# Optimization experiments

Measured on AMD Instinct MI355X. Metric: run time of the kernel, lower is better.

## Reference

```python
import jax, jax.numpy as jnp
import numpy as np

B, T, E = 8, 64, 512
H = 1024          # hidden_dim
OC = 2            # out_channels
VB = 32           # num_vel_bins
STEPS = 128


def setup_inputs() -> dict:
    key = jax.random.key(0)
    ks = jax.random.split(key, 16)
    s = 0.02
    f = lambda k, shp: jax.random.normal(k, shp, jnp.float32) * s
    return {
        "x": jax.random.normal(ks[0], (B, T, E), jnp.float32),
        "sos_token": f(ks[1], (1, 1, OC)),
        "Wc": f(ks[2], (E, H)), "bc": f(ks[3], (H,)),
        "Wi": f(ks[4], (OC, H)), "bi": f(ks[5], (H,)),
        "Wih0": f(ks[6], (2 * H, 4 * H)), "Whh0": f(ks[7], (H, 4 * H)),
        "bih0": f(ks[8], (4 * H,)), "bhh0": f(ks[9], (4 * H,)),
        "Wih1": f(ks[10], (H, 4 * H)), "Whh1": f(ks[11], (H, 4 * H)),
        "bih1": f(ks[12], (4 * H,)), "bhh1": f(ks[13], (4 * H,)),
        "Wo": f(ks[14], (H, 1 + VB)), "bo": f(ks[15], (1 + VB,)),
    }


def _lstm_cell(inp, h, c, Wih, Whh, b):
    # PyTorch gate order: i, f, g, o
    g = inp @ Wih + h @ Whh + b
    i, f, gg, o = jnp.split(g, 4, axis=-1)
    c = jax.nn.sigmoid(f) * c + jax.nn.sigmoid(i) * jnp.tanh(gg)
    h = jax.nn.sigmoid(o) * jnp.tanh(c)
    return h, c


def reference(x, sos_token, Wc, bc, Wi, bi, Wih0, Whh0, bih0, bhh0,
              Wih1, Whh1, bih1, bhh1, Wo, bo):
    Bx, Tx, Ex = x.shape
    BT = Bx * Tx
    Hd = Whh0.shape[0]
    nvb = Wo.shape[1] - 1
    cond = x.reshape(BT, Ex) @ Wc + bc            # [BT, H]
    b0 = bih0 + bhh0
    b1 = bih1 + bhh1
    z = jnp.zeros((BT, Hd), x.dtype)
    cur0 = jnp.broadcast_to(sos_token[0, 0], (BT, sos_token.shape[-1]))

    def step(carry, _):
        h0, c0, h1, c1, cur = carry
        inp = jnp.concatenate([cur @ Wi + bi, cond], axis=-1)  # [BT, 2H]
        h0, c0 = _lstm_cell(inp, h0, c0, Wih0, Whh0, b0)
        h1, c1 = _lstm_cell(h0, h1, c1, Wih1, Whh1, b1)
        logit = h1 @ Wo + bo                                   # [BT, 1+VB]
        pred_note = (jax.nn.sigmoid(logit[:, 0]) > 0.5).astype(x.dtype)
        pred_vel = jnp.argmax(logit[:, 1:], axis=-1).astype(x.dtype) / (nvb - 1.0)
        cur = jnp.stack([pred_note, pred_vel], axis=-1)        # [BT, 2]
        return (h0, c0, h1, c1, cur), logit

    _, logits = jax.lax.scan(step, (z, z, z, z, cur0), None, length=STEPS)
    # logits: [STEPS, BT, 1+VB] -> [B, 1+VB, T, 128]
    logits = logits.transpose(1, 0, 2).reshape(Bx, Tx, STEPS, 1 + nvb)
    return logits.transpose(0, 3, 1, 2)
```

## Files before the change

### kernel.cpp

```cpp
#include <hip/hip_runtime.h>
#include <hip/hip_bf16.h>


#define G4     4096
#define NSTEPS 128
#define NOUTC  33

typedef __attribute__((ext_vector_type(8))) short s8v;
typedef __attribute__((ext_vector_type(4))) float f4v;
typedef unsigned int u32;
typedef unsigned long long u64;

__device__ __forceinline__ float fsig(float x)  { return 1.0f / (1.0f + __expf(-x)); }
__device__ __forceinline__ float ftanh(float x) { return 2.0f / (1.0f + __expf(-2.0f * x)) - 1.0f; }

__device__ __forceinline__ short f2bf(float x) {
  union { __hip_bfloat16 b; short s; } u; u.b = __float2bfloat16(x); return u.s;
}
__device__ __forceinline__ float bf2f(short s) {
  union { __hip_bfloat16 b; short v; } u; u.v = s; return __bfloat162float(u.b);
}

__device__ __forceinline__ void gridbar(u32* bar, u32 target) {
  asm volatile("s_waitcnt vmcnt(0)" ::: "memory");
  __syncthreads();
  if (threadIdx.x == 0) {
    __hip_atomic_fetch_add(bar, 1u, __ATOMIC_RELAXED, __HIP_MEMORY_SCOPE_SYSTEM);
    while (__hip_atomic_load(bar, __ATOMIC_RELAXED, __HIP_MEMORY_SCOPE_SYSTEM) < target) {
      __builtin_amdgcn_s_sleep(1);
    }
  }
  __syncthreads();
}

__device__ __forceinline__ void stage16(short (*dst)[1032], const short* hbuf,
                                        int row0, int bankoff, int tid) {
#pragma unroll
  for (int i = 0; i < 8; ++i) {
    int q = i * 512 + tid;
    int row = q >> 8, c4 = q & 255;
    const u64* src = (const u64*)(hbuf + (size_t)(row0 + row) * G4 + bankoff) + c4;
    u64 v = __hip_atomic_load(src, __ATOMIC_RELAXED, __HIP_MEMORY_SCOPE_SYSTEM);
    *(u64*)&dst[row][c4 * 4] = v;
  }
}

__global__ __launch_bounds__(256) void transpose_frag_kernel(
    const float* __restrict__ src, short* __restrict__ dst_hi,
    short* __restrict__ dst_lo, int NK, int koff) {
  __shared__ float St[64][65];
  int n0 = (blockIdx.x & 63) * 64;
  int k0 = (blockIdx.x >> 6) * 64;
  int t = threadIdx.x;
  int nl = t & 63, kl = t >> 6;
#pragma unroll
  for (int it = 0; it < 16; ++it) {
    int k = kl + it * 4;
    St[k][nl] = src[(size_t)(k0 + k) * 4096 + n0 + nl];
  }
  __syncthreads();
  int lane = t & 63, w = t >> 6;
  for (int it = 0; it < 2; ++it) {
    int sub = it * 4 + w;
    int nt = sub >> 1, kc = sub & 1;
    int nloc = nt * 16 + (lane & 15);
    int kbase = kc * 32 + (lane >> 4) * 8;
    float v[8];
#pragma unroll
    for (int ii = 0; ii < 8; ++ii) v[ii] = St[kbase + ii][nloc];
    s8v hv;
#pragma unroll
    for (int ii = 0; ii < 8; ++ii) hv[ii] = f2bf(v[ii]);
    size_t ntg = (size_t)(n0 / 16 + nt);
    size_t kcg = (size_t)(k0 / 32 + kc + koff);
    size_t off = (ntg * (size_t)NK + kcg) * 512 + (size_t)lane * 8;
    *(s8v*)(dst_hi + off) = hv;
    if (dst_lo) {
      s8v lv;
#pragma unroll
      for (int ii = 0; ii < 8; ++ii) lv[ii] = f2bf(v[ii] - bf2f(hv[ii]));
      *(s8v*)(dst_lo + off) = lv;
    }
  }
}

__global__ __launch_bounds__(256) void cond_kernel(
    const float* __restrict__ x, const float* __restrict__ Wc,
    const float* __restrict__ bc, short* __restrict__ cond_hi,
    short* __restrict__ cond_lo) {
  __shared__ float xs[8][512];
  int rb = (blockIdx.x >> 2) * 8;
  int cb = (blockIdx.x & 3) * 256;
  int t = threadIdx.x;
  for (int i = t; i < 8 * 512; i += 256)
    xs[i >> 9][i & 511] = x[(size_t)(rb + (i >> 9)) * 512 + (i & 511)];
  __syncthreads();
  float acc[8] = {0, 0, 0, 0, 0, 0, 0, 0};
  for (int k = 0; k < 512; ++k) {
    float w = Wc[(size_t)k * 1024 + cb + t];
#pragma unroll
    for (int rr = 0; rr < 8; ++rr) acc[rr] += xs[rr][k] * w;
  }
  float bcv = bc[cb + t];
#pragma unroll
  for (int rr = 0; rr < 8; ++rr) {
    float v = acc[rr] + bcv;
    short hi = f2bf(v);
    cond_hi[(size_t)(rb + rr) * 1024 + cb + t] = hi;
    cond_lo[(size_t)(rb + rr) * 1024 + cb + t] = f2bf(v - bf2f(hi));
  }
}

__global__ __launch_bounds__(256) void vecs_kernel(
    const float* __restrict__ Wih0, const float* __restrict__ bi,
    const float* __restrict__ Wi, const float* __restrict__ bih0,
    const float* __restrict__ bhh0, const float* __restrict__ bih1,
    const float* __restrict__ bhh1, float* __restrict__ vec0,
    float* __restrict__ Wf, float* __restrict__ b1vec) {
  int n = blockIdx.x * 256 + threadIdx.x;
  float v0 = 0.f, w0 = 0.f, w1 = 0.f;
  for (int k = 0; k < 1024; ++k) {
    float w = Wih0[(size_t)k * 4096 + n];
    v0 += bi[k] * w;
    w0 += Wi[k] * w;
    w1 += Wi[1024 + k] * w;
  }
  vec0[n] = v0 + bih0[n] + bhh0[n];
  Wf[2 * n + 0] = w0;
  Wf[2 * n + 1] = w1;
  b1vec[n] = bih1[n] + bhh1[n];
}

__global__ __launch_bounds__(64) void wof_kernel(const float* __restrict__ Wo,
                                                 short* __restrict__ hi,
                                                 short* __restrict__ lo) {
  int nt = blockIdx.x >> 5;
  int kc = blockIdx.x & 31;
  int lane = threadIdx.x;
  int ch = nt * 16 + (lane & 15);
  int kb = kc * 32 + (lane >> 4) * 8;
  s8v hv, lv;
#pragma unroll
  for (int ii = 0; ii < 8; ++ii) {
    float v = (ch < NOUTC) ? Wo[(size_t)(kb + ii) * NOUTC + ch] : 0.f;
    short h = f2bf(v);
    hv[ii] = h;
    lv[ii] = f2bf(v - bf2f(h));
  }
  size_t off = ((size_t)(nt * 32 + kc)) * 512 + (size_t)lane * 8;
  *(s8v*)(hi + off) = hv;
  *(s8v*)(lo + off) = lv;
}

__global__ __launch_bounds__(512) void const0_kernel(
    const short* __restrict__ cond_hi, const short* __restrict__ cond_lo,
    const short* __restrict__ WTc_hi, const short* __restrict__ WTc_lo,
    const float* __restrict__ vec0, float* __restrict__ const0) {
  int j = blockIdx.x & 63, i = blockIdx.x >> 6;
  int w = threadIdx.x >> 6, lane = threadIdx.x & 63;
  int quad = lane >> 4, l16 = lane & 15;
  int rowA = i * 128 + w * 16 + l16;
  int rowC = i * 128 + w * 16 + quad * 4;
  int hid = j * 16 + l16;
  const short* ah = cond_hi + (size_t)rowA * 1024 + quad * 8;
  const short* al = cond_lo + (size_t)rowA * 1024 + quad * 8;
  f4v acc[4];
#pragma unroll
  for (int g = 0; g < 4; ++g) acc[g] = (f4v){0.f, 0.f, 0.f, 0.f};
#pragma unroll 2
  for (int kk = 0; kk < 32; ++kk) {
    s8v avh = *(const s8v*)(ah + kk * 32);
    s8v avl = *(const s8v*)(al + kk * 32);
#pragma unroll
    for (int g = 0; g < 4; ++g) {
      size_t off = ((size_t)(g * 64 + j) * 32 + kk) * 512 + (size_t)lane * 8;
      s8v bh = *(const s8v*)(WTc_hi + off);
      s8v bl = *(const s8v*)(WTc_lo + off);
      acc[g] = __builtin_amdgcn_mfma_f32_16x16x32_bf16(avh, bh, acc[g], 0, 0, 0);
      acc[g] = __builtin_amdgcn_mfma_f32_16x16x32_bf16(avh, bl, acc[g], 0, 0, 0);
      acc[g] = __builtin_amdgcn_mfma_f32_16x16x32_bf16(avl, bh, acc[g], 0, 0, 0);
    }
  }
#pragma unroll
  for (int g = 0; g < 4; ++g) {
    float vv = vec0[g * 1024 + hid];
#pragma unroll
    for (int p = 0; p < 4; ++p) {
      int r = rowC + p;
      const0[(size_t)r * G4 + g * 1024 + hid] = acc[g][p] + vv;
    }
  }
}

__global__ __launch_bounds__(512) void lstm_main(
    const short* __restrict__ WT0, const short* __restrict__ WT1,
    const float* __restrict__ const0, const float* __restrict__ Wf,
    const float* __restrict__ b1vec, const short* __restrict__ WoFh,
    const short* __restrict__ WoFl, const float* __restrict__ bo,
    const float* __restrict__ sos, float* __restrict__ out,
    short* __restrict__ hbuf, u32* __restrict__ bar) {
  int tid = threadIdx.x;
  u32 xcc;
  asm volatile("s_getreg_b32 %0, hwreg(20, 0, 32)" : "=s"(xcc));
  xcc &= 7;
  __shared__ u32 sslot;
  if (tid == 0)
    sslot = __hip_atomic_fetch_add(&bar[xcc], 1u, __ATOMIC_RELAXED,
                                   __HIP_MEMORY_SCOPE_SYSTEM);
  __syncthreads();
  u32 jb = sslot;
  if (jb >= 32) return;
  u32* gbar = bar + 64 + (size_t)jb * 16;

  int w = tid >> 6, lane = tid & 63;
  int g = w >> 1, half = w & 1;
  int quad = lane >> 4, l16 = lane & 15;
  int quad8 = quad * 8;
  int x = (int)xcc;
  int row0 = (int)jb * 16;
  int erow = tid >> 5;
  int ecb  = (tid & 31) * 4;
  int gr = row0 + erow;

  __shared__ short Ast[16][1032];
  __shared__ short Bst[16][1032];
  __shared__ float accst[4][16][132];
  __shared__ float lgl[16][34];
  __shared__ float curs[16][2];

  float wf0v[4][4], wf1v[4][4], b1vv[4][4], c0vv[4][4];
#pragma unroll
  for (int g2 = 0; g2 < 4; ++g2)
#pragma unroll
    for (int cc = 0; cc < 4; ++cc) {
      int n = g2 * 1024 + x * 128 + ecb + cc;
      wf0v[g2][cc] = Wf[2 * n + 0];
      wf1v[g2][cc] = Wf[2 * n + 1];
      b1vv[g2][cc] = b1vec[n];
      c0vv[g2][cc] = const0[(size_t)gr * G4 + n];
    }
  size_t nb0[4], nb1[4];
#pragma unroll
  for (int j = 0; j < 4; ++j) {
    int nt = g * 64 + x * 8 + half * 4 + j;
    nb0[j] = (size_t)nt * 32;
    nb1[j] = (size_t)nt * 64;
  }
  float boA = (w == 0) ? bo[l16] : ((w == 1) ? bo[16 + l16] : bo[32]);
  float sos0 = sos[0], sos1 = sos[1];
  float c0s[4] = {0.f, 0.f, 0.f, 0.f};
  float c1s[4] = {0.f, 0.f, 0.f, 0.f};
  u64 sink = 0;
  u32 snum = 0;

  for (int s = 0; s < NSTEPS; ++s) {
    int bank_r = (s & 1) * 2048;
    int bank_w = ((s + 1) & 1) * 2048;

    if (s > 0) {
      stage16(Ast, hbuf, row0, bank_r, tid);
      stage16(Bst, hbuf, row0, bank_r + 1024, tid);
      asm volatile("s_waitcnt vmcnt(0)" ::: "memory");
      __syncthreads();
      if (w < 3) {
        f4v la = {0.f, 0.f, 0.f, 0.f};
        const short* bh = WoFh + (size_t)w * 32 * 512 + (size_t)lane * 8;
        const short* bl = WoFl + (size_t)w * 32 * 512 + (size_t)lane * 8;
#pragma unroll 4
        for (int kk = 0; kk < 32; ++kk) {
          s8v av = *(const s8v*)&Bst[l16][quad8 + kk * 32];
          la = __builtin_amdgcn_mfma_f32_16x16x32_bf16(av, *(const s8v*)(bh + (size_t)kk * 512), la, 0, 0, 0);
          la = __builtin_amdgcn_mfma_f32_16x16x32_bf16(av, *(const s8v*)(bl + (size_t)kk * 512), la, 0, 0, 0);
        }
        int r0 = quad * 4;
#pragma unroll
        for (int p = 0; p < 4; ++p) {
          if (w == 0)      lgl[r0 + p][l16]      = la[p] + boA;
          else if (w == 1) lgl[r0 + p][16 + l16] = la[p] + boA;
          else if (l16 == 0) lgl[r0 + p][32]     = la[p] + boA;
        }
      }
    }
    {
      f4v acc[4];
#pragma unroll
      for (int j = 0; j < 4; ++j) acc[j] = (f4v){0.f, 0.f, 0.f, 0.f};
      if (s > 0) {
#pragma unroll 4
        for (int kk = 0; kk < 32; ++kk) {
          s8v av = *(const s8v*)&Ast[l16][quad8 + kk * 32];
#pragma unroll
          for (int j = 0; j < 4; ++j) {
            s8v bv = *(const s8v*)(WT0 + (nb0[j] + kk) * 512 + (size_t)lane * 8);
            acc[j] = __builtin_amdgcn_mfma_f32_16x16x32_bf16(av, bv, acc[j], 0, 0, 0);
          }
        }
      }
#pragma unroll
      for (int j = 0; j < 4; ++j)
#pragma unroll
        for (int p = 0; p < 4; ++p)
          accst[g][quad * 4 + p][(half * 4 + j) * 16 + l16] = acc[j][p];
    }
    __syncthreads();
    if (s > 0) {
      if (tid < 16) {
        float note = (lgl[tid][0] > 0.0f) ? 1.0f : 0.0f;
        float mx = lgl[tid][1];
        int mi = 0;
        for (int v = 1; v < 32; ++v) {
          float t = lgl[tid][1 + v];
          if (t > mx) { mx = t; mi = v; }
        }
        curs[tid][0] = note;
        curs[tid][1] = (float)mi * (1.0f / 31.0f);
      }
      if (xcc == 0) {
        for (int q = tid; q < 16 * NOUTC; q += 512) {
          int rl = q / NOUTC, chn = q - rl * NOUTC;
          int r = row0 + rl;
          out[((size_t)((r >> 6) * NOUTC + chn) * 64 + (r & 63)) * 128 + (s - 1)] =
              lgl[rl][chn];
        }
      }
    }
    __syncthreads();
    {
      float cu0v = (s == 0) ? sos0 : curs[erow][0];
      float cu1v = (s == 0) ? sos1 : curs[erow][1];
      f4v aI = *(const f4v*)&accst[0][erow][ecb];
      f4v aF = *(const f4v*)&accst[1][erow][ecb];
      f4v aG = *(const f4v*)&accst[2][erow][ecb];
      f4v aO = *(const f4v*)&accst[3][erow][ecb];
      union { u64 pk; short hv[4]; } u;
#pragma unroll
      for (int cc = 0; cc < 4; ++cc) {
        float gi = aI[cc] + c0vv[0][cc] + cu0v * wf0v[0][cc] + cu1v * wf1v[0][cc];
        float gf = aF[cc] + c0vv[1][cc] + cu0v * wf0v[1][cc] + cu1v * wf1v[1][cc];
        float gg = aG[cc] + c0vv[2][cc] + cu0v * wf0v[2][cc] + cu1v * wf1v[2][cc];
        float go = aO[cc] + c0vv[3][cc] + cu0v * wf0v[3][cc] + cu1v * wf1v[3][cc];
        float ccv = fsig(gf) * c0s[cc] + fsig(gi) * ftanh(gg);
        c0s[cc] = ccv;
        u.hv[cc] = f2bf(fsig(go) * ftanh(ccv));
      }
      u64* dst = (u64*)(hbuf + (size_t)gr * G4 + bank_w + x * 128 + ecb);
      sink ^= __hip_atomic_exchange(dst, u.pk, __ATOMIC_RELAXED,
                                    __HIP_MEMORY_SCOPE_SYSTEM);
    }
    ++snum; gridbar(gbar, snum * 8u);

    stage16(Ast, hbuf, row0, bank_w, tid);
    asm volatile("s_waitcnt vmcnt(0)" ::: "memory");
    __syncthreads();
    {
      f4v acc[4];
#pragma unroll
      for (int j = 0; j < 4; ++j) acc[j] = (f4v){0.f, 0.f, 0.f, 0.f};
#pragma unroll 4
      for (int kk = 0; kk < 32; ++kk) {
        s8v av = *(const s8v*)&Ast[l16][quad8 + kk * 32];
#pragma unroll
        for (int j = 0; j < 4; ++j) {
          s8v bv = *(const s8v*)(WT1 + (nb1[j] + kk) * 512 + (size_t)lane * 8);
          acc[j] = __builtin_amdgcn_mfma_f32_16x16x32_bf16(av, bv, acc[j], 0, 0, 0);
        }
      }
      if (s > 0) {
#pragma unroll 4
        for (int kk = 0; kk < 32; ++kk) {
          s8v av = *(const s8v*)&Bst[l16][quad8 + kk * 32];
#pragma unroll
          for (int j = 0; j < 4; ++j) {
            s8v bv = *(const s8v*)(WT1 + (nb1[j] + 32 + kk) * 512 + (size_t)lane * 8);
            acc[j] = __builtin_amdgcn_mfma_f32_16x16x32_bf16(av, bv, acc[j], 0, 0, 0);
          }
        }
      }
#pragma unroll
      for (int j = 0; j < 4; ++j)
#pragma unroll
        for (int p = 0; p < 4; ++p)
          accst[g][quad * 4 + p][(half * 4 + j) * 16 + l16] = acc[j][p];
    }
    __syncthreads();
    {
      f4v aI = *(const f4v*)&accst[0][erow][ecb];
      f4v aF = *(const f4v*)&accst[1][erow][ecb];
      f4v aG = *(const f4v*)&accst[2][erow][ecb];
      f4v aO = *(const f4v*)&accst[3][erow][ecb];
      union { u64 pk; short hv[4]; } u;
#pragma unroll
      for (int cc = 0; cc < 4; ++cc) {
        float gi = aI[cc] + b1vv[0][cc];
        float gf = aF[cc] + b1vv[1][cc];
        float gg = aG[cc] + b1vv[2][cc];
        float go = aO[cc] + b1vv[3][cc];
        float ccv = fsig(gf) * c1s[cc] + fsig(gi) * ftanh(gg);
        c1s[cc] = ccv;
        u.hv[cc] = f2bf(fsig(go) * ftanh(ccv));
      }
      u64* dst = (u64*)(hbuf + (size_t)gr * G4 + bank_w + 1024 + x * 128 + ecb);
      sink ^= __hip_atomic_exchange(dst, u.pk, __ATOMIC_RELAXED,
                                    __HIP_MEMORY_SCOPE_SYSTEM);
    }
    ++snum; gridbar(gbar, snum * 8u);
  }

  if (xcc == 0) {
    stage16(Bst, hbuf, row0, 0 + 1024, tid);
    asm volatile("s_waitcnt vmcnt(0)" ::: "memory");
    __syncthreads();
    if (w < 3) {
      f4v la = {0.f, 0.f, 0.f, 0.f};
      const short* bh = WoFh + (size_t)w * 32 * 512 + (size_t)lane * 8;
      const short* bl = WoFl + (size_t)w * 32 * 512 + (size_t)lane * 8;
#pragma unroll 4
      for (int kk = 0; kk < 32; ++kk) {
        s8v av = *(const s8v*)&Bst[l16][quad8 + kk * 32];
        la = __builtin_amdgcn_mfma_f32_16x16x32_bf16(av, *(const s8v*)(bh + (size_t)kk * 512), la, 0, 0, 0);
        la = __builtin_amdgcn_mfma_f32_16x16x32_bf16(av, *(const s8v*)(bl + (size_t)kk * 512), la, 0, 0, 0);
      }
      int r0 = quad * 4;
#pragma unroll
      for (int p = 0; p < 4; ++p) {
        if (w == 0)      lgl[r0 + p][l16]      = la[p] + boA;
        else if (w == 1) lgl[r0 + p][16 + l16] = la[p] + boA;
        else if (l16 == 0) lgl[r0 + p][32]     = la[p] + boA;
      }
    }
    __syncthreads();
    for (int q = tid; q < 16 * NOUTC; q += 512) {
      int rl = q / NOUTC, chn = q - rl * NOUTC;
      int r = row0 + rl;
      out[((size_t)((r >> 6) * NOUTC + chn) * 64 + (r & 63)) * 128 + (NSTEPS - 1)] =
          lgl[rl][chn];
    }
  }
  asm volatile("" :: "v"(sink));
}

extern "C" void kernel_launch(void* const* d_in, const int* in_sizes, int n_in,
                              void* d_out, int out_size, void* d_ws, size_t ws_size,
                              hipStream_t stream) {
  (void)in_sizes; (void)n_in; (void)out_size; (void)ws_size;
  const float* x    = (const float*)d_in[0];
  const float* sos  = (const float*)d_in[1];
  const float* Wc   = (const float*)d_in[2];
  const float* bc   = (const float*)d_in[3];
  const float* Wi   = (const float*)d_in[4];
  const float* bi   = (const float*)d_in[5];
  const float* Wih0 = (const float*)d_in[6];
  const float* Whh0 = (const float*)d_in[7];
  const float* bih0 = (const float*)d_in[8];
  const float* bhh0 = (const float*)d_in[9];
  const float* Wih1 = (const float*)d_in[10];
  const float* Whh1 = (const float*)d_in[11];
  const float* bih1 = (const float*)d_in[12];
  const float* bhh1 = (const float*)d_in[13];
  const float* Wo   = (const float*)d_in[14];
  const float* bo   = (const float*)d_in[15];
  float* out = (float*)d_out;

  char* p = (char*)d_ws;
  short* WT0    = (short*)p; p += (size_t)256 * 32 * 512 * 2;
  short* WT1    = (short*)p; p += (size_t)256 * 64 * 512 * 2;
  short* WTc_hi = (short*)p; p += (size_t)256 * 32 * 512 * 2;
  short* WTc_lo = (short*)p; p += (size_t)256 * 32 * 512 * 2;
  float* const0 = (float*)p; p += (size_t)512 * 4096 * 4;
  short* hbuf   = (short*)p; p += (size_t)512 * 4096 * 2;
  short* cond_hi= (short*)p; p += (size_t)512 * 1024 * 2;
  short* cond_lo= (short*)p; p += (size_t)512 * 1024 * 2;
  float* vec0   = (float*)p; p += 4096 * 4;
  float* Wf     = (float*)p; p += 4096 * 2 * 4;
  float* b1vec  = (float*)p; p += 4096 * 4;
  short* WoFh   = (short*)p; p += (size_t)48 * 1024 * 2;
  short* WoFl   = (short*)p; p += (size_t)48 * 1024 * 2;
  u32*   bar    = (u32*)p;   p += 4096;

  hipMemsetAsync(bar, 0, 4096, stream);

  transpose_frag_kernel<<<1024, 256, 0, stream>>>(Whh0, WT0, nullptr, 32, 0);
  transpose_frag_kernel<<<1024, 256, 0, stream>>>(Wih1, WT1, nullptr, 64, 0);
  transpose_frag_kernel<<<1024, 256, 0, stream>>>(Whh1, WT1, nullptr, 64, 32);
  transpose_frag_kernel<<<1024, 256, 0, stream>>>(Wih0 + (size_t)1024 * 4096,
                                                  WTc_hi, WTc_lo, 32, 0);
  cond_kernel<<<256, 256, 0, stream>>>(x, Wc, bc, cond_hi, cond_lo);
  vecs_kernel<<<16, 256, 0, stream>>>(Wih0, bi, Wi, bih0, bhh0, bih1, bhh1,
                                      vec0, Wf, b1vec);
  wof_kernel<<<96, 64, 0, stream>>>(Wo, WoFh, WoFl);
  const0_kernel<<<256, 512, 0, stream>>>(cond_hi, cond_lo, WTc_hi, WTc_lo,
                                         vec0, const0);
  lstm_main<<<2048, 512, 0, stream>>>(WT0, WT1, const0, Wf, b1vec, WoFh, WoFl,
                                      bo, sos, out, hbuf, bar);
}
```

Measured before the change: 6.546 ms.

## Overlap hidden-state staging with layer-0 MFMA and drop redundant Ast reload

At the start of each step, the layer-1 hidden state (Bst) is no longer staged synchronously together with a redundant reload of Ast, which the previous step had already staged from the same bank. Instead, 16-byte global loads with sc0 sc1 cache bits are issued into registers before the layer-0 MFMA loop and written to LDS afterwards. The output-projection matmul is moved after that write. This aims to hide global-memory latency in the serialized recurrent step and cut load instructions, at the cost of extra vector registers and inline asm whose coherence relies on the sc bits.

```diff
diff --git a/kernel.cpp b/kernel.cpp
--- a/kernel.cpp
+++ b/kernel.cpp
@@ -33,15 +33,24 @@
   __syncthreads();
 }
 
-__device__ __forceinline__ void stage16(short (*dst)[1032], const short* hbuf,
-                                        int row0, int bankoff, int tid) {
-#pragma unroll
-  for (int i = 0; i < 8; ++i) {
+__device__ __forceinline__ void stage_issue(const short* hbuf, int row0,
+                                            int bankoff, int tid, s8v* r) {
+#pragma unroll
+  for (int i = 0; i < 4; ++i) {
     int q = i * 512 + tid;
-    int row = q >> 8, c4 = q & 255;
-    const u64* src = (const u64*)(hbuf + (size_t)(row0 + row) * G4 + bankoff) + c4;
-    u64 v = __hip_atomic_load(src, __ATOMIC_RELAXED, __HIP_MEMORY_SCOPE_SYSTEM);
-    *(u64*)&dst[row][c4 * 4] = v;
+    int row = q >> 7, c16 = q & 127;
+    const short* src = hbuf + (size_t)(row0 + row) * G4 + bankoff + c16 * 8;
+    asm volatile("global_load_dwordx4 %0, %1, off sc0 sc1"
+                 : "=&v"(r[i]) : "v"(src) : "memory");
+  }
+}
+__device__ __forceinline__ void stage_write(short (*dst)[1032], int tid,
+                                            const s8v* r) {
+#pragma unroll
+  for (int i = 0; i < 4; ++i) {
+    int q = i * 512 + tid;
+    int row = q >> 7, c16 = q & 127;
+    *(s8v*)&dst[row][c16 * 8] = r[i];
   }
 }
 
@@ -256,31 +265,11 @@
   for (int s = 0; s < NSTEPS; ++s) {
     int bank_r = (s & 1) * 2048;
     int bank_w = ((s + 1) & 1) * 2048;
-
-    if (s > 0) {
-      stage16(Ast, hbuf, row0, bank_r, tid);
-      stage16(Bst, hbuf, row0, bank_r + 1024, tid);
-      asm volatile("s_waitcnt vmcnt(0)" ::: "memory");
-      __syncthreads();
-      if (w < 3) {
-        f4v la = {0.f, 0.f, 0.f, 0.f};
-        const short* bh = WoFh + (size_t)w * 32 * 512 + (size_t)lane * 8;
-        const short* bl = WoFl + (size_t)w * 32 * 512 + (size_t)lane * 8;
-#pragma unroll 4
-        for (int kk = 0; kk < 32; ++kk) {
-          s8v av = *(const s8v*)&Bst[l16][quad8 + kk * 32];
-          la = __builtin_amdgcn_mfma_f32_16x16x32_bf16(av, *(const s8v*)(bh + (size_t)kk * 512), la, 0, 0, 0);
-          la = __builtin_amdgcn_mfma_f32_16x16x32_bf16(av, *(const s8v*)(bl + (size_t)kk * 512), la, 0, 0, 0);
-        }
-        int r0 = quad * 4;
-#pragma unroll
-        for (int p = 0; p < 4; ++p) {
-          if (w == 0)      lgl[r0 + p][l16]      = la[p] + boA;
-          else if (w == 1) lgl[r0 + p][16 + l16] = la[p] + boA;
-          else if (l16 == 0) lgl[r0 + p][32]     = la[p] + boA;
-        }
-      }
-    }
+    s8v breg[4];
+
+    if (s > 0)
+      stage_issue(hbuf, row0, bank_r + 1024, tid, breg);
+
     {
       f4v acc[4];
 #pragma unroll
@@ -301,6 +290,30 @@
 #pragma unroll
         for (int p = 0; p < 4; ++p)
           accst[g][quad * 4 + p][(half * 4 + j) * 16 + l16] = acc[j][p];
+    }
+    if (s > 0) {
+      asm volatile("s_waitcnt vmcnt(0)" ::: "memory");
+      __builtin_amdgcn_sched_barrier(0);
+      stage_write(Bst, tid, breg);
+    }
+    __syncthreads();
+    if (s > 0 && w < 3) {
+      f4v la = {0.f, 0.f, 0.f, 0.f};
+      const short* bh = WoFh + (size_t)w * 32 * 512 + (size_t)lane * 8;
+      const short* bl = WoFl + (size_t)w * 32 * 512 + (size_t)lane * 8;
+#pragma unroll 4
+      for (int kk = 0; kk < 32; ++kk) {
+        s8v av = *(const s8v*)&Bst[l16][quad8 + kk * 32];
+        la = __builtin_amdgcn_mfma_f32_16x16x32_bf16(av, *(const s8v*)(bh + (size_t)kk * 512), la, 0, 0, 0);
+        la = __builtin_amdgcn_mfma_f32_16x16x32_bf16(av, *(const s8v*)(bl + (size_t)kk * 512), la, 0, 0, 0);
+      }
+      int r0 = quad * 4;
+#pragma unroll
+      for (int p = 0; p < 4; ++p) {
+        if (w == 0)      lgl[r0 + p][l16]      = la[p] + boA;
+        else if (w == 1) lgl[r0 + p][16 + l16] = la[p] + boA;
+        else if (l16 == 0) lgl[r0 + p][32]     = la[p] + boA;
+      }
     }
     __syncthreads();
     if (s > 0) {
@@ -349,8 +362,10 @@
     }
     ++snum; gridbar(gbar, snum * 8u);
 
-    stage16(Ast, hbuf, row0, bank_w, tid);
+    stage_issue(hbuf, row0, bank_w, tid, breg);
     asm volatile("s_waitcnt vmcnt(0)" ::: "memory");
+    __builtin_amdgcn_sched_barrier(0);
+    stage_write(Ast, tid, breg);
     __syncthreads();
     {
       f4v acc[4];
@@ -407,8 +422,11 @@
   }
 
   if (xcc == 0) {
-    stage16(Bst, hbuf, row0, 0 + 1024, tid);
+    s8v breg[4];
+    stage_issue(hbuf, row0, 0 + 1024, tid, breg);
     asm volatile("s_waitcnt vmcnt(0)" ::: "memory");
+    __builtin_amdgcn_sched_barrier(0);
+    stage_write(Bst, tid, breg);
     __syncthreads();
     if (w < 3) {
       f4v la = {0.f, 0.f, 0.f, 0.f};
```

Measured after the change: 6.188 ms. 5.5% less time.
